# Optimization experiments

Hardware: AMD Instinct MI355X
Metric: run time of the kernel (lower is better)

The kernel has to match this reference:

```python
import jax, jax.numpy as jnp
import numpy as np

N_TOKENS = 8192
D_MODEL = 1024
D_HIDDEN = 4096
N_EXPERTS = 8
TOP_K = 2


def setup_inputs() -> dict:
    key = jax.random.key(0)
    ks = jax.random.split(key, 7)
    s = 0.02
    return {
        "x": jax.random.normal(ks[0], (N_TOKENS, D_MODEL), dtype=jnp.float32),
        "gate_w": jax.random.normal(ks[1], (D_MODEL, N_EXPERTS), dtype=jnp.float32) * s,
        "gate_b": jnp.zeros((N_EXPERTS,), dtype=jnp.float32),
        "w1": jax.random.normal(ks[2], (N_EXPERTS, D_MODEL, D_HIDDEN), dtype=jnp.float32) * s,
        "b1": jnp.zeros((N_EXPERTS, D_HIDDEN), dtype=jnp.float32),
        "w2": jax.random.normal(ks[3], (N_EXPERTS, D_HIDDEN, D_MODEL), dtype=jnp.float32) * s,
        "b2": jnp.zeros((N_EXPERTS, D_MODEL), dtype=jnp.float32),
    }


def reference(x, gate_w, gate_b, w1, b1, w2, b2):
    # Gating: softmax over experts, then top-k routing
    gate_scores = jax.nn.softmax(x @ gate_w + gate_b, axis=-1)        # [N, E]
    topk_vals, topk_idx = jax.lax.top_k(gate_scores, TOP_K)          # [N, K]

    # Combine weights: sum of topk_vals scattered to expert slots
    onehot = jax.nn.one_hot(topk_idx, N_EXPERTS, dtype=x.dtype)      # [N, K, E]
    combine = jnp.einsum('nk,nke->ne', topk_vals, onehot)            # [N, E]

    # Dense expert evaluation (math identical to masked dispatch: unselected
    # experts receive weight 0 in `combine`).
    h = jax.nn.relu(jnp.einsum('nd,edh->neh', x, w1) + b1)           # [N, E, H]
    expert_out = jnp.einsum('neh,ehd->ned', h, w2) + b2              # [N, E, D]
    output = jnp.einsum('ned,ne->nd', expert_out, combine)           # [N, D]

    # Load-balancing loss from routing counts
    load = jnp.sum(onehot, axis=(0, 1))                              # [E]
    load_balancing_loss = jnp.sum((load / jnp.sum(load)) ** 2)
    return output, load_balancing_loss
```

## Files before the change

### kernel.cpp

```cpp
#include <hip/hip_runtime.h>

#define D_MODEL   1024
#define D_HIDDEN  4096
#define N_EXPERTS 8
#define N_TOKENS  8192
#define NASSIGN   (N_TOKENS * 2)
#define PADCAP    (NASSIGN + N_EXPERTS * 128)
#define ROWT      (PADCAP / 128)

typedef unsigned short u16;
typedef __bf16 bf16x8 __attribute__((ext_vector_type(8)));
typedef float  f32x4  __attribute__((ext_vector_type(4)));

__device__ __forceinline__ u16 f2bf(float f) {
  union { float f; unsigned u; } c; c.f = f;
  unsigned u = c.u;
  u = (u + 0x7fffu + ((u >> 16) & 1u)) >> 16;
  return (u16)u;
}

__device__ __forceinline__ void async16(const void* g, void* l) {
  __builtin_amdgcn_global_load_lds(
      (const __attribute__((address_space(1))) unsigned int*)g,
      (__attribute__((address_space(3))) unsigned int*)l, 16, 0, 0);
}

__global__ __launch_bounds__(256) void gating_kernel(
    const float* __restrict__ x, const float* __restrict__ gw,
    const float* __restrict__ gb, int* __restrict__ counts,
    int* __restrict__ tok_idx, float* __restrict__ tok_w,
    u16* __restrict__ xb)
{
  const int n = blockIdx.x * 4 + (threadIdx.x >> 6);
  const int lane = threadIdx.x & 63;
  const float4* x4 = (const float4*)x;
  const float4* gw4 = (const float4*)gw;

  float acc[8] = {0.f,0.f,0.f,0.f,0.f,0.f,0.f,0.f};
  #pragma unroll
  for (int cch = 0; cch < 4; ++cch) {
    const int f4i = cch * 64 + lane;
    float4 xv = x4[(size_t)n * 256 + f4i];

    uint2 o;
    o.x = (unsigned)f2bf(xv.x) | ((unsigned)f2bf(xv.y) << 16);
    o.y = (unsigned)f2bf(xv.z) | ((unsigned)f2bf(xv.w) << 16);
    *(uint2*)&xb[(size_t)n * D_MODEL + f4i * 4] = o;

    float xr[4] = {xv.x, xv.y, xv.z, xv.w};
    #pragma unroll
    for (int r = 0; r < 4; ++r) {
      int row = f4i * 4 + r;
      float4 g0 = gw4[row * 2], g1 = gw4[row * 2 + 1];
      acc[0] += xr[r] * g0.x; acc[1] += xr[r] * g0.y;
      acc[2] += xr[r] * g0.z; acc[3] += xr[r] * g0.w;
      acc[4] += xr[r] * g1.x; acc[5] += xr[r] * g1.y;
      acc[6] += xr[r] * g1.z; acc[7] += xr[r] * g1.w;
    }
  }
  for (int off = 32; off; off >>= 1)
    #pragma unroll
    for (int e = 0; e < 8; ++e) acc[e] += __shfl_xor(acc[e], off, 64);
  if (lane == 0) {
    float l[8], p[8];
    float m = -1e30f;
    for (int e = 0; e < 8; ++e) { l[e] = acc[e] + gb[e]; m = fmaxf(m, l[e]); }
    float s = 0.f;
    for (int e = 0; e < 8; ++e) { p[e] = expf(l[e] - m); s += p[e]; }
    float inv = 1.f / s;
    for (int e = 0; e < 8; ++e) p[e] *= inv;
    int i0 = 0;
    for (int e = 1; e < 8; ++e) if (p[e] > p[i0]) i0 = e;
    int i1 = (i0 == 0) ? 1 : 0;
    for (int e = 0; e < 8; ++e) if (e != i0 && p[e] > p[i1]) i1 = e;
    tok_idx[2 * n]     = i0;  tok_idx[2 * n + 1] = i1;
    tok_w[2 * n]       = p[i0]; tok_w[2 * n + 1] = p[i1];
    atomicAdd(&counts[i0], 1);
    atomicAdd(&counts[i1], 1);
  }
}

__global__ void finalize_routing(const int* __restrict__ counts,
                                 int* __restrict__ offsets,
                                 float* __restrict__ out_loss)
{
  int off = 0;
  for (int e = 0; e < 8; ++e) {
    offsets[e] = off;
    off += ((counts[e] + 127) >> 7) << 7;
  }
  offsets[8] = off;
  float loss = 0.f;
  for (int e = 0; e < 8; ++e) {
    float f = (float)counts[e] * (1.f / (float)NASSIGN);
    loss += f * f;
  }
  *out_loss = loss;
}

__global__ __launch_bounds__(256) void scatter_kernel(
    const int* __restrict__ tok_idx, const float* __restrict__ tok_w,
    const int* __restrict__ offsets, int* __restrict__ cursors,
    int* __restrict__ assign_token, float* __restrict__ assign_w,
    int* __restrict__ tok_pos)
{
  const int n = blockIdx.x * 256 + threadIdx.x;
  #pragma unroll
  for (int k = 0; k < 2; ++k) {
    int e = tok_idx[n * 2 + k];
    int pos = offsets[e] + atomicAdd(&cursors[e], 1);
    assign_token[pos] = n;
    assign_w[pos] = tok_w[n * 2 + k];
    tok_pos[n * 2 + k] = pos;
  }
}

__global__ __launch_bounds__(256) void transpose_cvt_kernel(
    const float* __restrict__ in, u16* __restrict__ out, int R, int C)
{
  const int e = blockIdx.z;
  const int c0 = blockIdx.x * 64, r0 = blockIdx.y * 64;
  __shared__ float tile[64][65];
  const int tx = threadIdx.x & 15;
  const int ty = threadIdx.x >> 4;
  const float* ip = in + (size_t)e * R * C;
  u16* op = out + (size_t)e * R * C;
  #pragma unroll
  for (int i = 0; i < 4; ++i) {
    int r = ty + i * 16;
    float4 v = *(const float4*)&ip[(size_t)(r0 + r) * C + c0 + tx * 4];
    tile[r][tx * 4 + 0] = v.x; tile[r][tx * 4 + 1] = v.y;
    tile[r][tx * 4 + 2] = v.z; tile[r][tx * 4 + 3] = v.w;
  }
  __syncthreads();
  const int c = threadIdx.x >> 2, seg = threadIdx.x & 3;
  u16 buf[16];
  #pragma unroll
  for (int k = 0; k < 16; ++k) buf[k] = f2bf(tile[seg * 16 + k][c]);
  *(uint4*)&op[(size_t)(c0 + c) * R + r0 + seg * 16]     = *(const uint4*)&buf[0];
  *(uint4*)&op[(size_t)(c0 + c) * R + r0 + seg * 16 + 8] = *(const uint4*)&buf[8];
}


__global__ __launch_bounds__(256, 2) void gemm1_kernel(
    const u16* __restrict__ xb, const u16* __restrict__ w1t,
    const float* __restrict__ b1, const int* __restrict__ assign_token,
    const int* __restrict__ offsets, u16* __restrict__ hbuf)
{
  const int rt = (blockIdx.x & 7) * 17 + (blockIdx.x >> 3);
  const int ct = blockIdx.y;
  if (rt * 128 >= offsets[8]) return;
  int e = 0;
  while (offsets[e + 1] <= rt * 128) ++e;

  __shared__ __align__(16) u16 smem[36864];
  u16* Asm = smem;
  u16* Bsm = smem + 12288;

  const int tid = threadIdx.x;
  const int wave = tid >> 6, lane = tid & 63;

  const int ra0 = tid >> 2,         sa = tid & 3;
  const int ra1 = (tid + 256) >> 2;
  const int sga0 = sa ^ ((ra0 >> 1) & 3);
  const int sga1 = sa ^ ((ra1 >> 1) & 3);
  const long aBase0 = (long)assign_token[rt * 128 + ra0] * D_MODEL + sga0 * 8;
  const long aBase1 = (long)assign_token[rt * 128 + ra1] * D_MODEL + sga1 * 8;

  long bBase[4];
  #pragma unroll
  for (int k = 0; k < 4; ++k) {
    int c = tid + k * 256;
    int r = c >> 2, s = c & 3;
    int sg = s ^ ((r >> 1) & 3);
    bBase[k] = ((long)e * D_HIDDEN + ct * 256 + r) * D_MODEL + sg * 8;
  }

  const int wr = (wave >> 1) * 64;
  const int wc = (wave & 1) * 128;
  f32x4 acc[4][8];
  #pragma unroll
  for (int i = 0; i < 4; ++i)
    #pragma unroll
    for (int j = 0; j < 8; ++j) acc[i][j] = (f32x4){0.f, 0.f, 0.f, 0.f};

  int aoff[4], boff[8];
  #pragma unroll
  for (int i = 0; i < 4; ++i) {
    int row = wr + i * 16 + (lane & 15);
    aoff[i] = row * 32 + (((lane >> 4) ^ ((row >> 1) & 3)) * 8);
  }
  #pragma unroll
  for (int j = 0; j < 8; ++j) {
    int col = wc + j * 16 + (lane & 15);
    boff[j] = col * 32 + (((lane >> 4) ^ ((col >> 1) & 3)) * 8);
  }

  #define STAGE1(bi, k0) do { \
    u16* A_ = Asm + (bi) * 4096; \
    u16* B_ = Bsm + (bi) * 8192; \
    async16(xb  + aBase0   + (k0), A_ + wave * 512); \
    async16(xb  + aBase1   + (k0), A_ + 2048 + wave * 512); \
    async16(w1t + bBase[0] + (k0), B_ + wave * 512); \
    async16(w1t + bBase[1] + (k0), B_ + 2048 + wave * 512); \
    async16(w1t + bBase[2] + (k0), B_ + 4096 + wave * 512); \
    async16(w1t + bBase[3] + (k0), B_ + 6144 + wave * 512); \
  } while (0)

  const int NT = D_MODEL / 32;
  STAGE1(0, 0);
  STAGE1(1, 32);
  int bi = 0;
  for (int t = 0; t < NT; ++t) {
    if (t < NT - 1) asm volatile("s_waitcnt vmcnt(6)" ::: "memory");
    else            asm volatile("s_waitcnt vmcnt(0)" ::: "memory");
    __builtin_amdgcn_s_barrier();
    const u16* A = Asm + bi * 4096;
    const u16* B = Bsm + bi * 8192;
    bf16x8 a[4], b[8];
    #pragma unroll
    for (int i = 0; i < 4; ++i) a[i] = *(const bf16x8*)&A[aoff[i]];
    #pragma unroll
    for (int j = 0; j < 8; ++j) b[j] = *(const bf16x8*)&B[boff[j]];
    __builtin_amdgcn_s_setprio(1);
    #pragma unroll
    for (int i = 0; i < 4; ++i)
      #pragma unroll
      for (int j = 0; j < 8; ++j)
        acc[i][j] = __builtin_amdgcn_mfma_f32_16x16x32_bf16(a[i], b[j], acc[i][j], 0, 0, 0);
    __builtin_amdgcn_s_setprio(0);
    if (t + 2 < NT) {
      int nb = bi + 2; if (nb >= 3) nb -= 3;
      STAGE1(nb, (t + 2) * 32);
    }
    ++bi; if (bi == 3) bi = 0;
  }
  #undef STAGE1

  float bias[8];
  #pragma unroll
  for (int j = 0; j < 8; ++j)
    bias[j] = b1[(size_t)e * D_HIDDEN + ct * 256 + wc + j * 16 + (lane & 15)];

  __syncthreads();
  u16* Hs = smem;
  #pragma unroll
  for (int i = 0; i < 4; ++i)
    #pragma unroll
    for (int j = 0; j < 8; ++j)
      #pragma unroll
      for (int r = 0; r < 4; ++r) {
        int rl = wr + i * 16 + ((lane >> 4) * 4) + r;
        int cl = wc + j * 16 + (lane & 15);
        Hs[rl * 256 + cl] = f2bf(fmaxf(acc[i][j][r] + bias[j], 0.f));
      }
  __syncthreads();
  #pragma unroll
  for (int t = 0; t < 16; ++t) {
    int cc = tid + t * 256;
    int row = cc >> 5, cs = cc & 31;
    *(uint4*)&hbuf[((size_t)(rt * 128 + row)) * D_HIDDEN + ct * 256 + cs * 8] =
        *(const uint4*)&Hs[row * 256 + cs * 8];
  }
}

template <bool EO>
__global__ __launch_bounds__(256, 2) void gemm2_kernel(
    const u16* __restrict__ hbuf, const u16* __restrict__ w2t,
    const float* __restrict__ b2, const int* __restrict__ assign_token,
    const float* __restrict__ assign_w, const int* __restrict__ offsets,
    float* __restrict__ dst)
{
  const int rt = (blockIdx.x & 7) * 17 + (blockIdx.x >> 3);
  const int ct = blockIdx.y;
  if (rt * 128 >= offsets[8]) return;
  int e = 0;
  while (offsets[e + 1] <= rt * 128) ++e;

  __shared__ __align__(16) u16 smem[36864];
  u16* Asm = smem;
  u16* Bsm = smem + 12288;
  __shared__ int tokS[128];
  __shared__ float wS[128];

  const int tid = threadIdx.x;
  const int wave = tid >> 6, lane = tid & 63;
  if (tid < 128) {
    tokS[tid] = assign_token[rt * 128 + tid];
    wS[tid] = assign_w[rt * 128 + tid];
  }

  const int ra0 = tid >> 2,         sa = tid & 3;
  const int ra1 = (tid + 256) >> 2;
  const int sga0 = sa ^ ((ra0 >> 1) & 3);
  const int sga1 = sa ^ ((ra1 >> 1) & 3);
  const long aBase0 = ((long)(rt * 128 + ra0)) * D_HIDDEN + sga0 * 8;
  const long aBase1 = ((long)(rt * 128 + ra1)) * D_HIDDEN + sga1 * 8;

  long bBase[4];
  #pragma unroll
  for (int k = 0; k < 4; ++k) {
    int c = tid + k * 256;
    int r = c >> 2, s = c & 3;
    int sg = s ^ ((r >> 1) & 3);
    bBase[k] = ((long)e * D_MODEL + ct * 256 + r) * D_HIDDEN + sg * 8;
  }

  const int wr = (wave >> 1) * 64;
  const int wc = (wave & 1) * 128;
  f32x4 acc[4][8];
  #pragma unroll
  for (int i = 0; i < 4; ++i)
    #pragma unroll
    for (int j = 0; j < 8; ++j) acc[i][j] = (f32x4){0.f, 0.f, 0.f, 0.f};

  int aoff[4], boff[8];
  #pragma unroll
  for (int i = 0; i < 4; ++i) {
    int row = wr + i * 16 + (lane & 15);
    aoff[i] = row * 32 + (((lane >> 4) ^ ((row >> 1) & 3)) * 8);
  }
  #pragma unroll
  for (int j = 0; j < 8; ++j) {
    int col = wc + j * 16 + (lane & 15);
    boff[j] = col * 32 + (((lane >> 4) ^ ((col >> 1) & 3)) * 8);
  }

  #define STAGE2(bi, k0) do { \
    u16* A_ = Asm + (bi) * 4096; \
    u16* B_ = Bsm + (bi) * 8192; \
    async16(hbuf + aBase0   + (k0), A_ + wave * 512); \
    async16(hbuf + aBase1   + (k0), A_ + 2048 + wave * 512); \
    async16(w2t  + bBase[0] + (k0), B_ + wave * 512); \
    async16(w2t  + bBase[1] + (k0), B_ + 2048 + wave * 512); \
    async16(w2t  + bBase[2] + (k0), B_ + 4096 + wave * 512); \
    async16(w2t  + bBase[3] + (k0), B_ + 6144 + wave * 512); \
  } while (0)

  const int NT = D_HIDDEN / 32;
  STAGE2(0, 0);
  STAGE2(1, 32);
  int bi = 0;
  for (int t = 0; t < NT; ++t) {
    if (t < NT - 1) asm volatile("s_waitcnt vmcnt(6)" ::: "memory");
    else            asm volatile("s_waitcnt vmcnt(0)" ::: "memory");
    __builtin_amdgcn_s_barrier();
    const u16* A = Asm + bi * 4096;
    const u16* B = Bsm + bi * 8192;
    bf16x8 a[4], b[8];
    #pragma unroll
    for (int i = 0; i < 4; ++i) a[i] = *(const bf16x8*)&A[aoff[i]];
    #pragma unroll
    for (int j = 0; j < 8; ++j) b[j] = *(const bf16x8*)&B[boff[j]];
    __builtin_amdgcn_s_setprio(1);
    #pragma unroll
    for (int i = 0; i < 4; ++i)
      #pragma unroll
      for (int j = 0; j < 8; ++j)
        acc[i][j] = __builtin_amdgcn_mfma_f32_16x16x32_bf16(a[i], b[j], acc[i][j], 0, 0, 0);
    __builtin_amdgcn_s_setprio(0);
    if (t + 2 < NT) {
      int nb = bi + 2; if (nb >= 3) nb -= 3;
      STAGE2(nb, (t + 2) * 32);
    }
    ++bi; if (bi == 3) bi = 0;
  }
  #undef STAGE2

  float bias[8];
  #pragma unroll
  for (int j = 0; j < 8; ++j)
    bias[j] = b2[(size_t)e * D_MODEL + ct * 256 + wc + j * 16 + (lane & 15)];

  #pragma unroll
  for (int i = 0; i < 4; ++i)
    #pragma unroll
    for (int r = 0; r < 4; ++r) {
      int rl = wr + i * 16 + ((lane >> 4) * 4) + r;
      float wgt = wS[rl];
      if (EO) {
        size_t row = (size_t)(rt * 128 + rl);
        #pragma unroll
        for (int j = 0; j < 8; ++j) {
          float v = (acc[i][j][r] + bias[j]) * wgt;
          dst[row * D_MODEL + ct * 256 + wc + j * 16 + (lane & 15)] = v;
        }
      } else {
        int tok = tokS[rl];
        #pragma unroll
        for (int j = 0; j < 8; ++j) {
          float v = (acc[i][j][r] + bias[j]) * wgt;
          atomicAdd(&dst[(size_t)tok * D_MODEL + ct * 256 + wc + j * 16 + (lane & 15)], v);
        }
      }
    }
}

__global__ __launch_bounds__(256) void combine_kernel(
    const float* __restrict__ eo, const int* __restrict__ tok_pos,
    float* __restrict__ out)
{
  int idx = blockIdx.x * 256 + threadIdx.x;
  int n = idx >> 8;
  int c = (idx & 255) * 4;
  int p0 = tok_pos[2 * n], p1 = tok_pos[2 * n + 1];
  float4 a = *(const float4*)&eo[(size_t)p0 * D_MODEL + c];
  float4 b = *(const float4*)&eo[(size_t)p1 * D_MODEL + c];
  float4 o; o.x = a.x + b.x; o.y = a.y + b.y; o.z = a.z + b.z; o.w = a.w + b.w;
  *(float4*)&out[(size_t)n * D_MODEL + c] = o;
}

__global__ __launch_bounds__(256) void moe_fallback_kernel(
    const float* __restrict__ x, const float* __restrict__ w1,
    const float* __restrict__ b1, const float* __restrict__ w2,
    const float* __restrict__ b2, const int* __restrict__ tok_idx,
    const float* __restrict__ tok_w, float* __restrict__ out)
{
  const int a = blockIdx.x;
  const int n = a >> 1, slot = a & 1;
  const int e = tok_idx[n * 2 + slot];
  const float wgt = tok_w[n * 2 + slot];
  __shared__ float xs[D_MODEL];
  __shared__ float hs[D_HIDDEN];
  const int tid = threadIdx.x;
  for (int d = tid; d < D_MODEL; d += 256) xs[d] = x[(size_t)n * D_MODEL + d];
  __syncthreads();
  for (int h = tid; h < D_HIDDEN; h += 256) {
    float acc = b1[(size_t)e * D_HIDDEN + h];
    for (int d = 0; d < D_MODEL; ++d)
      acc += xs[d] * w1[((size_t)e * D_MODEL + d) * D_HIDDEN + h];
    hs[h] = fmaxf(acc, 0.f);
  }
  __syncthreads();
  for (int d = tid; d < D_MODEL; d += 256) {
    float acc = b2[(size_t)e * D_MODEL + d];
    for (int h = 0; h < D_HIDDEN; ++h)
      acc += hs[h] * w2[((size_t)e * D_HIDDEN + h) * D_MODEL + d];
    atomicAdd(&out[(size_t)n * D_MODEL + d], wgt * acc);
  }
}

extern "C" void kernel_launch(void* const* d_in, const int* in_sizes, int n_in,
                              void* d_out, int out_size, void* d_ws, size_t ws_size,
                              hipStream_t stream) {
  const float* x      = (const float*)d_in[0];
  const float* gate_w = (const float*)d_in[1];
  const float* gate_b = (const float*)d_in[2];
  const float* w1     = (const float*)d_in[3];
  const float* b1     = (const float*)d_in[4];
  const float* w2     = (const float*)d_in[5];
  const float* b2     = (const float*)d_in[6];
  float* out = (float*)d_out;

  char* ws = (char*)d_ws;
  int*   counts       = (int*)(ws + 0);
  int*   cursors      = (int*)(ws + 32);
  int*   offsets      = (int*)(ws + 64);
  int*   tok_idx      = (int*)(ws + 256);
  float* tok_w        = (float*)(ws + 65792);
  int*   tok_pos      = (int*)(ws + 131328);
  int*   assign_token = (int*)(ws + 196864);
  float* assign_w     = (float*)(ws + 266496);
  const size_t X0 = 336128;
  u16* xb   = (u16*)(ws + X0);
  u16* w1t  = (u16*)(ws + X0 + 16777216);
  u16* w2t  = (u16*)(ws + X0);
  u16* hbuf = (u16*)(ws + X0 + 83886080);
  float* eo = (float*)(ws + X0 + 226492416ull);
  const size_t REQ_FAST = X0 + 226492416ull;
  const size_t REQ_EO   = REQ_FAST + 71303168ull;

  const bool fast = (ws_size >= REQ_FAST);
  const bool eoPath = (ws_size >= REQ_EO);

  hipMemsetAsync(ws, 0, fast ? X0 : 336128, stream);
  if (!eoPath) {
    hipMemsetAsync(d_out, 0, (size_t)out_size * sizeof(float), stream);
  }

  gating_kernel<<<N_TOKENS / 4, 256, 0, stream>>>(x, gate_w, gate_b, counts,
                                                  tok_idx, tok_w, xb);
  finalize_routing<<<1, 1, 0, stream>>>(counts, offsets, out + (out_size - 1));

  if (fast) {
    scatter_kernel<<<N_TOKENS / 256, 256, 0, stream>>>(tok_idx, tok_w, offsets, cursors,
                                                       assign_token, assign_w, tok_pos);
    transpose_cvt_kernel<<<dim3(D_HIDDEN / 64, D_MODEL / 64, N_EXPERTS), 256, 0, stream>>>(
        w1, w1t, D_MODEL, D_HIDDEN);
    gemm1_kernel<<<dim3(ROWT, D_HIDDEN / 256), 256, 0, stream>>>(
        xb, w1t, b1, assign_token, offsets, hbuf);
    transpose_cvt_kernel<<<dim3(D_MODEL / 64, D_HIDDEN / 64, N_EXPERTS), 256, 0, stream>>>(
        w2, w2t, D_HIDDEN, D_MODEL);
    if (eoPath) {
      gemm2_kernel<true><<<dim3(ROWT, D_MODEL / 256), 256, 0, stream>>>(
          hbuf, w2t, b2, assign_token, assign_w, offsets, eo);
      combine_kernel<<<(N_TOKENS * D_MODEL) / 1024, 256, 0, stream>>>(eo, tok_pos, out);
    } else {
      gemm2_kernel<false><<<dim3(ROWT, D_MODEL / 256), 256, 0, stream>>>(
          hbuf, w2t, b2, assign_token, assign_w, offsets, out);
    }
  } else {
    moe_fallback_kernel<<<NASSIGN, 256, 0, stream>>>(x, w1, b1, w2, b2, tok_idx, tok_w, out);
  }
}
```

Before: 749.3 us.

## Store expert outputs as bf16 and retile weight transpose for wider stores

The intermediate expert-output buffer written by the second GEMM and read by the combine kernel changes from fp32 to bf16, which halves that round-trip traffic and the workspace it needs. The weight transpose-and-convert kernel moves to 256x32 tiles, so each thread writes 16-byte rows of bf16 along the longer dimension. The cost is an extra bf16 rounding of each weighted expert output before the two are summed, which slightly lowers output precision. The smaller workspace requirement also makes the expert-output path available with less workspace.

```diff
diff --git a/kernel.cpp b/kernel.cpp
--- a/kernel.cpp
+++ b/kernel.cpp
@@ -17,6 +17,11 @@
   unsigned u = c.u;
   u = (u + 0x7fffu + ((u >> 16) & 1u)) >> 16;
   return (u16)u;
+}
+
+__device__ __forceinline__ float bf2f(u16 v) {
+  union { unsigned u; float f; } c; c.u = ((unsigned)v) << 16;
+  return c.f;
 }
 
 __device__ __forceinline__ void async16(const void* g, void* l) {
@@ -119,26 +124,29 @@
     const float* __restrict__ in, u16* __restrict__ out, int R, int C)
 {
   const int e = blockIdx.z;
-  const int c0 = blockIdx.x * 64, r0 = blockIdx.y * 64;
-  __shared__ float tile[64][65];
-  const int tx = threadIdx.x & 15;
-  const int ty = threadIdx.x >> 4;
+  const int c0 = blockIdx.x * 32, r0 = blockIdx.y * 256;
+  __shared__ float tile[256][34];
+  const int tid = threadIdx.x;
   const float* ip = in + (size_t)e * R * C;
   u16* op = out + (size_t)e * R * C;
-  #pragma unroll
-  for (int i = 0; i < 4; ++i) {
-    int r = ty + i * 16;
-    float4 v = *(const float4*)&ip[(size_t)(r0 + r) * C + c0 + tx * 4];
-    tile[r][tx * 4 + 0] = v.x; tile[r][tx * 4 + 1] = v.y;
-    tile[r][tx * 4 + 2] = v.z; tile[r][tx * 4 + 3] = v.w;
+  const int rr = tid >> 3, cc4 = (tid & 7) * 4;
+  #pragma unroll
+  for (int p = 0; p < 8; ++p) {
+    int r = rr + p * 32;
+    float4 v = *(const float4*)&ip[(size_t)(r0 + r) * C + c0 + cc4];
+    tile[r][cc4 + 0] = v.x; tile[r][cc4 + 1] = v.y;
+    tile[r][cc4 + 2] = v.z; tile[r][cc4 + 3] = v.w;
   }
   __syncthreads();
-  const int c = threadIdx.x >> 2, seg = threadIdx.x & 3;
-  u16 buf[16];
-  #pragma unroll
-  for (int k = 0; k < 16; ++k) buf[k] = f2bf(tile[seg * 16 + k][c]);
-  *(uint4*)&op[(size_t)(c0 + c) * R + r0 + seg * 16]     = *(const uint4*)&buf[0];
-  *(uint4*)&op[(size_t)(c0 + c) * R + r0 + seg * 16 + 8] = *(const uint4*)&buf[8];
+  const int c = tid >> 5, ch = tid & 31;
+  #pragma unroll
+  for (int p = 0; p < 4; ++p) {
+    int crow = c + p * 8;
+    u16 buf[8];
+    #pragma unroll
+    for (int j = 0; j < 8; ++j) buf[j] = f2bf(tile[ch * 8 + j][crow]);
+    *(uint4*)&op[(size_t)(c0 + crow) * R + r0 + ch * 8] = *(const uint4*)&buf[0];
+  }
 }
 
 
@@ -269,7 +277,7 @@
     const u16* __restrict__ hbuf, const u16* __restrict__ w2t,
     const float* __restrict__ b2, const int* __restrict__ assign_token,
     const float* __restrict__ assign_w, const int* __restrict__ offsets,
-    float* __restrict__ dst)
+    void* __restrict__ dstv)
 {
   const int rt = (blockIdx.x & 7) * 17 + (blockIdx.x >> 3);
   const int ct = blockIdx.y;
@@ -379,13 +387,15 @@
       int rl = wr + i * 16 + ((lane >> 4) * 4) + r;
       float wgt = wS[rl];
       if (EO) {
+        u16* dst = (u16*)dstv;
         size_t row = (size_t)(rt * 128 + rl);
         #pragma unroll
         for (int j = 0; j < 8; ++j) {
           float v = (acc[i][j][r] + bias[j]) * wgt;
-          dst[row * D_MODEL + ct * 256 + wc + j * 16 + (lane & 15)] = v;
+          dst[row * D_MODEL + ct * 256 + wc + j * 16 + (lane & 15)] = f2bf(v);
         }
       } else {
+        float* dst = (float*)dstv;
         int tok = tokS[rl];
         #pragma unroll
         for (int j = 0; j < 8; ++j) {
@@ -397,16 +407,20 @@
 }
 
 __global__ __launch_bounds__(256) void combine_kernel(
-    const float* __restrict__ eo, const int* __restrict__ tok_pos,
+    const u16* __restrict__ eo, const int* __restrict__ tok_pos,
     float* __restrict__ out)
 {
   int idx = blockIdx.x * 256 + threadIdx.x;
   int n = idx >> 8;
   int c = (idx & 255) * 4;
   int p0 = tok_pos[2 * n], p1 = tok_pos[2 * n + 1];
-  float4 a = *(const float4*)&eo[(size_t)p0 * D_MODEL + c];
-  float4 b = *(const float4*)&eo[(size_t)p1 * D_MODEL + c];
-  float4 o; o.x = a.x + b.x; o.y = a.y + b.y; o.z = a.z + b.z; o.w = a.w + b.w;
+  uint2 ua = *(const uint2*)&eo[(size_t)p0 * D_MODEL + c];
+  uint2 ub = *(const uint2*)&eo[(size_t)p1 * D_MODEL + c];
+  float4 o;
+  o.x = bf2f((u16)(ua.x & 0xffff))  + bf2f((u16)(ub.x & 0xffff));
+  o.y = bf2f((u16)(ua.x >> 16))     + bf2f((u16)(ub.x >> 16));
+  o.z = bf2f((u16)(ua.y & 0xffff))  + bf2f((u16)(ub.y & 0xffff));
+  o.w = bf2f((u16)(ua.y >> 16))     + bf2f((u16)(ub.y >> 16));
   *(float4*)&out[(size_t)n * D_MODEL + c] = o;
 }
 
@@ -466,9 +480,9 @@
   u16* w1t  = (u16*)(ws + X0 + 16777216);
   u16* w2t  = (u16*)(ws + X0);
   u16* hbuf = (u16*)(ws + X0 + 83886080);
-  float* eo = (float*)(ws + X0 + 226492416ull);
+  u16* eo   = (u16*)(ws + X0 + 226492416ull);
   const size_t REQ_FAST = X0 + 226492416ull;
-  const size_t REQ_EO   = REQ_FAST + 71303168ull;
+  const size_t REQ_EO   = REQ_FAST + 35651584ull;
 
   const bool fast = (ws_size >= REQ_FAST);
   const bool eoPath = (ws_size >= REQ_EO);
@@ -485,11 +499,11 @@
   if (fast) {
     scatter_kernel<<<N_TOKENS / 256, 256, 0, stream>>>(tok_idx, tok_w, offsets, cursors,
                                                        assign_token, assign_w, tok_pos);
-    transpose_cvt_kernel<<<dim3(D_HIDDEN / 64, D_MODEL / 64, N_EXPERTS), 256, 0, stream>>>(
+    transpose_cvt_kernel<<<dim3(D_HIDDEN / 32, D_MODEL / 256, N_EXPERTS), 256, 0, stream>>>(
         w1, w1t, D_MODEL, D_HIDDEN);
     gemm1_kernel<<<dim3(ROWT, D_HIDDEN / 256), 256, 0, stream>>>(
         xb, w1t, b1, assign_token, offsets, hbuf);
-    transpose_cvt_kernel<<<dim3(D_MODEL / 64, D_HIDDEN / 64, N_EXPERTS), 256, 0, stream>>>(
+    transpose_cvt_kernel<<<dim3(D_MODEL / 32, D_HIDDEN / 256, N_EXPERTS), 256, 0, stream>>>(
         w2, w2t, D_HIDDEN, D_MODEL);
     if (eoPath) {
       gemm2_kernel<true><<<dim3(ROWT, D_MODEL / 256), 256, 0, stream>>>(
```

Result: no change. 739.4 us (-1.3%).

## Store gemm2 expert outputs in bf16 and double-buffer LDS for occupancy

Applied to the files above, without the earlier changes.

Expert outputs in the EO path are now written as bf16 instead of fp32, halving the intermediate buffer and the traffic through the combine kernel. Combine unpacks bf16 pairs back to float before summing. Gemm2 moves from a triple-buffered LDS pipeline to a double-buffered one, with an extra barrier before issuing the next prefetch, so LDS use drops and launch bounds can ask for 3 blocks per CU. This adds bf16 rounding error to the outputs, and the extra barrier may expose more load latency.

```diff
diff --git a/kernel.cpp b/kernel.cpp
--- a/kernel.cpp
+++ b/kernel.cpp
@@ -17,6 +17,11 @@
   unsigned u = c.u;
   u = (u + 0x7fffu + ((u >> 16) & 1u)) >> 16;
   return (u16)u;
+}
+
+__device__ __forceinline__ float bf2f(u16 v) {
+  union { unsigned u; float f; } c; c.u = ((unsigned)v) << 16;
+  return c.f;
 }
 
 __device__ __forceinline__ void async16(const void* g, void* l) {
@@ -141,7 +146,6 @@
   *(uint4*)&op[(size_t)(c0 + c) * R + r0 + seg * 16 + 8] = *(const uint4*)&buf[8];
 }
 
-
 __global__ __launch_bounds__(256, 2) void gemm1_kernel(
     const u16* __restrict__ xb, const u16* __restrict__ w1t,
     const float* __restrict__ b1, const int* __restrict__ assign_token,
@@ -265,11 +269,11 @@
 }
 
 template <bool EO>
-__global__ __launch_bounds__(256, 2) void gemm2_kernel(
+__global__ __launch_bounds__(256, 3) void gemm2_kernel(
     const u16* __restrict__ hbuf, const u16* __restrict__ w2t,
     const float* __restrict__ b2, const int* __restrict__ assign_token,
     const float* __restrict__ assign_w, const int* __restrict__ offsets,
-    float* __restrict__ dst)
+    void* __restrict__ dstv)
 {
   const int rt = (blockIdx.x & 7) * 17 + (blockIdx.x >> 3);
   const int ct = blockIdx.y;
@@ -277,9 +281,7 @@
   int e = 0;
   while (offsets[e + 1] <= rt * 128) ++e;
 
-  __shared__ __align__(16) u16 smem[36864];
-  u16* Asm = smem;
-  u16* Bsm = smem + 12288;
+  __shared__ __align__(16) u16 smem[24576];
   __shared__ int tokS[128];
   __shared__ float wS[128];
 
@@ -327,8 +329,8 @@
   }
 
   #define STAGE2(bi, k0) do { \
-    u16* A_ = Asm + (bi) * 4096; \
-    u16* B_ = Bsm + (bi) * 8192; \
+    u16* A_ = smem + (bi) * 12288; \
+    u16* B_ = A_ + 4096; \
     async16(hbuf + aBase0   + (k0), A_ + wave * 512); \
     async16(hbuf + aBase1   + (k0), A_ + 2048 + wave * 512); \
     async16(w2t  + bBase[0] + (k0), B_ + wave * 512); \
@@ -340,18 +342,19 @@
   const int NT = D_HIDDEN / 32;
   STAGE2(0, 0);
   STAGE2(1, 32);
-  int bi = 0;
   for (int t = 0; t < NT; ++t) {
+    const u16* A = smem + (t & 1) * 12288;
+    const u16* B = A + 4096;
     if (t < NT - 1) asm volatile("s_waitcnt vmcnt(6)" ::: "memory");
     else            asm volatile("s_waitcnt vmcnt(0)" ::: "memory");
     __builtin_amdgcn_s_barrier();
-    const u16* A = Asm + bi * 4096;
-    const u16* B = Bsm + bi * 8192;
     bf16x8 a[4], b[8];
     #pragma unroll
     for (int i = 0; i < 4; ++i) a[i] = *(const bf16x8*)&A[aoff[i]];
     #pragma unroll
     for (int j = 0; j < 8; ++j) b[j] = *(const bf16x8*)&B[boff[j]];
+    asm volatile("s_waitcnt lgkmcnt(0)\n\ts_barrier" ::: "memory");
+    if (t + 2 < NT) STAGE2(t & 1, (t + 2) * 32);
     __builtin_amdgcn_s_setprio(1);
     #pragma unroll
     for (int i = 0; i < 4; ++i)
@@ -359,11 +362,6 @@
       for (int j = 0; j < 8; ++j)
         acc[i][j] = __builtin_amdgcn_mfma_f32_16x16x32_bf16(a[i], b[j], acc[i][j], 0, 0, 0);
     __builtin_amdgcn_s_setprio(0);
-    if (t + 2 < NT) {
-      int nb = bi + 2; if (nb >= 3) nb -= 3;
-      STAGE2(nb, (t + 2) * 32);
-    }
-    ++bi; if (bi == 3) bi = 0;
   }
   #undef STAGE2
 
@@ -379,13 +377,15 @@
       int rl = wr + i * 16 + ((lane >> 4) * 4) + r;
       float wgt = wS[rl];
       if (EO) {
+        u16* dst = (u16*)dstv;
         size_t row = (size_t)(rt * 128 + rl);
         #pragma unroll
         for (int j = 0; j < 8; ++j) {
           float v = (acc[i][j][r] + bias[j]) * wgt;
-          dst[row * D_MODEL + ct * 256 + wc + j * 16 + (lane & 15)] = v;
+          dst[row * D_MODEL + ct * 256 + wc + j * 16 + (lane & 15)] = f2bf(v);
         }
       } else {
+        float* dst = (float*)dstv;
         int tok = tokS[rl];
         #pragma unroll
         for (int j = 0; j < 8; ++j) {
@@ -397,16 +397,20 @@
 }
 
 __global__ __launch_bounds__(256) void combine_kernel(
-    const float* __restrict__ eo, const int* __restrict__ tok_pos,
+    const u16* __restrict__ eo, const int* __restrict__ tok_pos,
     float* __restrict__ out)
 {
   int idx = blockIdx.x * 256 + threadIdx.x;
   int n = idx >> 8;
   int c = (idx & 255) * 4;
   int p0 = tok_pos[2 * n], p1 = tok_pos[2 * n + 1];
-  float4 a = *(const float4*)&eo[(size_t)p0 * D_MODEL + c];
-  float4 b = *(const float4*)&eo[(size_t)p1 * D_MODEL + c];
-  float4 o; o.x = a.x + b.x; o.y = a.y + b.y; o.z = a.z + b.z; o.w = a.w + b.w;
+  uint2 ua = *(const uint2*)&eo[(size_t)p0 * D_MODEL + c];
+  uint2 ub = *(const uint2*)&eo[(size_t)p1 * D_MODEL + c];
+  float4 o;
+  o.x = bf2f((u16)(ua.x & 0xffff))  + bf2f((u16)(ub.x & 0xffff));
+  o.y = bf2f((u16)(ua.x >> 16))     + bf2f((u16)(ub.x >> 16));
+  o.z = bf2f((u16)(ua.y & 0xffff))  + bf2f((u16)(ub.y & 0xffff));
+  o.w = bf2f((u16)(ua.y >> 16))     + bf2f((u16)(ub.y >> 16));
   *(float4*)&out[(size_t)n * D_MODEL + c] = o;
 }
 
@@ -466,9 +470,9 @@
   u16* w1t  = (u16*)(ws + X0 + 16777216);
   u16* w2t  = (u16*)(ws + X0);
   u16* hbuf = (u16*)(ws + X0 + 83886080);
-  float* eo = (float*)(ws + X0 + 226492416ull);
+  u16* eo   = (u16*)(ws + X0 + 226492416ull);
   const size_t REQ_FAST = X0 + 226492416ull;
-  const size_t REQ_EO   = REQ_FAST + 71303168ull;
+  const size_t REQ_EO   = REQ_FAST + 35651584ull;
 
   const bool fast = (ws_size >= REQ_FAST);
   const bool eoPath = (ws_size >= REQ_EO);
```

Measured after the change: 1.198 ms. 1.6x slower.
